# Optimization experiments

Hardware: AMD Instinct MI355X
Metric: run time of the kernel (lower is better)

The kernel has to match this reference:

```python
import jax, jax.numpy as jnp
import numpy as np


def setup_inputs() -> dict:
    key = jax.random.key(0)
    k1, k2 = jax.random.split(key)
    B, S, D = 16, 4096, 512
    xs = jax.random.normal(k1, (B, S, D), dtype=jnp.float32)
    # lengths in [1, S] so the mean is always well-defined (torch would NaN on 0)
    xs_len = jax.random.randint(k2, (B,), 1, S + 1, dtype=jnp.int64)
    return {"xs": xs, "xs_len": xs_len}


def reference(xs, xs_len):
    # Masked mean over the first xs_len[b] positions of each sequence.
    # Equivalent to torch.stack([x[:l].mean(dim=-2) for x, l in zip(xs, xs_len)])
    B, S, D = xs.shape
    mask = (jnp.arange(S)[None, :] < xs_len[:, None])  # [B, S]
    summed = jnp.einsum('bsd,bs->bd', xs, mask.astype(xs.dtype))  # [B, D]
    return summed / xs_len.astype(xs.dtype)[:, None]
```

## Files before the change

### kernel.cpp

```cpp
#include <hip/hip_runtime.h>
#include <hip/hip_bf16.h>


#define THREADS 128
#define CHUNKS  64

__global__ __launch_bounds__(THREADS) void mean_embed_kernel(
    const float* __restrict__ xs,
    const int*   __restrict__ xs_len,
    float*       __restrict__ out,
    int S, int D)
{
    const int b     = blockIdx.x;
    const int chunk = blockIdx.y;
    const int L     = xs_len[b];

    const int rows_per_blk = S / CHUNKS;
    const int row0 = chunk * rows_per_blk;
    if (row0 >= L) return;
    const int row1 = min(row0 + rows_per_blk, L);

    const int tid = threadIdx.x;
    const int d4  = D >> 2;

    const float4* base = (const float4*)(xs + (size_t)b * S * D);

    float4 acc = make_float4(0.f, 0.f, 0.f, 0.f);
    for (int s = row0; s < row1; ++s) {
        float4 v = base[(size_t)s * d4 + tid];
        acc.x += v.x; acc.y += v.y; acc.z += v.z; acc.w += v.w;
    }

    const float inv = 1.0f / (float)L;
    float* o = out + (size_t)b * D + tid * 4;
    atomicAdd(o + 0, acc.x * inv);
    atomicAdd(o + 1, acc.y * inv);
    atomicAdd(o + 2, acc.z * inv);
    atomicAdd(o + 3, acc.w * inv);
}

extern "C" void kernel_launch(void* const* d_in, const int* in_sizes, int n_in,
                              void* d_out, int out_size, void* d_ws, size_t ws_size,
                              hipStream_t stream) {
    const float* xs     = (const float*)d_in[0];
    const int*   xs_len = (const int*)d_in[1];
    float*       out    = (float*)d_out;

    const int B = in_sizes[1];
    const int total = in_sizes[0];
    const int D = 512;
    const int S = total / (B * D);

    hipMemsetAsync(d_out, 0, (size_t)out_size * sizeof(float), stream);

    dim3 grid(B, CHUNKS);
    mean_embed_kernel<<<grid, THREADS, 0, stream>>>(xs, xs_len, out, S, D);
}
```

Measured before the change: 198.0 us.

## Replace atomic accumulation with two-phase workspace reduction and more chunks

Splits the masked mean into two kernels. Phase one writes per-chunk partial sums to a workspace, with twice as many chunks and an unrolled row loop. Phase two sums the active chunks and writes the output with a plain store. This removes the memset and the float atomics and raises parallelism for the bandwidth-bound read. In exchange it adds a second launch and a small workspace round-trip.

```diff
diff --git a/kernel.cpp b/kernel.cpp
--- a/kernel.cpp
+++ b/kernel.cpp
@@ -3,22 +3,22 @@
 
 
 #define THREADS 128
-#define CHUNKS  64
+#define CHUNKS  128
 
-__global__ __launch_bounds__(THREADS) void mean_embed_kernel(
+__global__ __launch_bounds__(THREADS) void mean_embed_phase1(
     const float* __restrict__ xs,
     const int*   __restrict__ xs_len,
-    float*       __restrict__ out,
+    float*       __restrict__ ws,
     int S, int D)
 {
     const int b     = blockIdx.x;
     const int chunk = blockIdx.y;
     const int L     = xs_len[b];
 
-    const int rows_per_blk = S / CHUNKS;
-    const int row0 = chunk * rows_per_blk;
+    const int rows = S / CHUNKS;
+    const int row0 = chunk * rows;
     if (row0 >= L) return;
-    const int row1 = min(row0 + rows_per_blk, L);
+    const int row1 = min(row0 + rows, L);
 
     const int tid = threadIdx.x;
     const int d4  = D >> 2;
@@ -26,17 +26,40 @@
     const float4* base = (const float4*)(xs + (size_t)b * S * D);
 
     float4 acc = make_float4(0.f, 0.f, 0.f, 0.f);
+    #pragma unroll 4
     for (int s = row0; s < row1; ++s) {
         float4 v = base[(size_t)s * d4 + tid];
         acc.x += v.x; acc.y += v.y; acc.z += v.z; acc.w += v.w;
     }
 
+    float4* wsv = (float4*)ws;
+    wsv[((size_t)b * CHUNKS + chunk) * d4 + tid] = acc;
+}
+
+__global__ __launch_bounds__(THREADS) void mean_embed_phase2(
+    const float* __restrict__ ws,
+    const int*   __restrict__ xs_len,
+    float*       __restrict__ out,
+    int S, int D)
+{
+    const int b   = blockIdx.x;
+    const int tid = threadIdx.x;
+    const int L   = xs_len[b];
+    const int d4  = D >> 2;
+
+    const int rows   = S / CHUNKS;
+    const int nact   = (L + rows - 1) / rows;
+
+    const float4* wsv = (const float4*)ws;
+    float4 acc = make_float4(0.f, 0.f, 0.f, 0.f);
+    for (int c = 0; c < nact; ++c) {
+        float4 v = wsv[((size_t)b * CHUNKS + c) * d4 + tid];
+        acc.x += v.x; acc.y += v.y; acc.z += v.z; acc.w += v.w;
+    }
+
     const float inv = 1.0f / (float)L;
-    float* o = out + (size_t)b * D + tid * 4;
-    atomicAdd(o + 0, acc.x * inv);
-    atomicAdd(o + 1, acc.y * inv);
-    atomicAdd(o + 2, acc.z * inv);
-    atomicAdd(o + 3, acc.w * inv);
+    float4 r = make_float4(acc.x * inv, acc.y * inv, acc.z * inv, acc.w * inv);
+    ((float4*)out)[(size_t)b * d4 + tid] = r;
 }
 
 extern "C" void kernel_launch(void* const* d_in, const int* in_sizes, int n_in,
@@ -45,14 +68,14 @@
     const float* xs     = (const float*)d_in[0];
     const int*   xs_len = (const int*)d_in[1];
     float*       out    = (float*)d_out;
+    float*       ws     = (float*)d_ws;
 
     const int B = in_sizes[1];
     const int total = in_sizes[0];
     const int D = 512;
     const int S = total / (B * D);
 
-    hipMemsetAsync(d_out, 0, (size_t)out_size * sizeof(float), stream);
-
-    dim3 grid(B, CHUNKS);
-    mean_embed_kernel<<<grid, THREADS, 0, stream>>>(xs, xs_len, out, S, D);
+    dim3 g1(B, CHUNKS);
+    mean_embed_phase1<<<g1, THREADS, 0, stream>>>(xs, xs_len, ws, S, D);
+    mean_embed_phase2<<<B, THREADS, 0, stream>>>(ws, xs_len, out, S, D);
 }
```

Measured after the change: 203.9 us. 1.03x slower.
